# Kernel optimization log

Measured on AMD Instinct MI355X. Metric: run time of the kernel, lower is better.

The kernel has to match this reference:

```python
import jax, jax.numpy as jnp
import numpy as np

# Config (mirrors MarketBDHConfig / BDHConfig defaults used here)
B, T = 2, 512
NUM_ASSETS, IN_FEAT = 93, 4
D = 256          # n_embd
NH = 4           # n_head
MULT = 64        # mlp_internal_dim_multiplier
NL = 6           # n_layer
NI = D * MULT // NH  # per-head internal dim N = 4096
IN_DIM = NUM_ASSETS * IN_FEAT  # 372
ROPE_THETA = 2.0 ** 16
EPS = 1e-5


def _ln(x):
    # LayerNorm over last dim, elementwise_affine=False
    m = jnp.mean(x, axis=-1, keepdims=True)
    v = jnp.mean(jnp.square(x - m), axis=-1, keepdims=True)
    return (x - m) * jax.lax.rsqrt(v + EPS)


def _rope(x, cos, sin):
    # x: [B,NH,T,NI]; cos/sin: [T, NI//2] (broadcast over B,NH)
    x1, x2 = x[..., 0::2], x[..., 1::2]
    out = jnp.stack([x1 * cos - x2 * sin, x1 * sin + x2 * cos], axis=-1)
    return out.reshape(x.shape)


def setup_inputs() -> dict:
    key = jax.random.key(0)
    ks = jax.random.split(key, 9)
    s = 0.02
    return {
        "x": jax.random.normal(ks[0], (B, T, NUM_ASSETS, IN_FEAT), jnp.float32),
        "in_W": jax.random.normal(ks[1], (IN_DIM, D), jnp.float32) * s,
        "in_b": jnp.zeros((D,), jnp.float32),
        "encoder": jax.random.normal(ks[2], (NH, D, NI), jnp.float32) * s,
        "encoder_v": jax.random.normal(ks[3], (NH, D, NI), jnp.float32) * s,
        "decoder": jax.random.normal(ks[4], (NH * NI, D), jnp.float32) * s,
        "head_W": jax.random.normal(ks[5], (D, IN_DIM), jnp.float32) * s,
        "head_b": jnp.zeros((IN_DIM,), jnp.float32),
    }


def reference(x, in_W, in_b, encoder, encoder_v, decoder, head_W, head_b):
    # input projection: [B,T,N,F] -> [B,T,IN_DIM] -> [B,T,D]
    x_flat = x.reshape(B, T, IN_DIM)
    h = _ln(x_flat @ in_W + in_b)  # [B,T,D]

    # RoPE phase tables over the internal (latent) dimension
    freqs = 1.0 / (ROPE_THETA ** (jnp.arange(0, NI, 2, dtype=jnp.float32) / NI))
    phases = jnp.arange(T, dtype=jnp.float32)[:, None] * freqs[None, :]  # [T, NI/2]
    cos, sin = jnp.cos(phases), jnp.sin(phases)

    dec = decoder.reshape(NH, NI, D)  # head-major flatten matches transpose(1,2).reshape

    for _ in range(NL):
        h_res = h
        # encode + relu-sparsify: [B,NH,T,NI]
        h_sparse = jax.nn.relu(jnp.einsum('btd,hdn->bhtn', h, encoder))
        # BDH attention: linear (no softmax), K is Q, is_causal=False -> dense scores
        qr = _rope(h_sparse, cos, sin)
        scores = jnp.einsum('bhtn,bhsn->bhts', qr, qr)  # [B,NH,T,T]
        yKV = jnp.einsum('bhts,bsd->bhtd', scores, h)    # V = h broadcast over heads
        yKV = _ln(yKV)
        y_sparse = jax.nn.relu(jnp.einsum('bhtd,hdn->bhtn', yKV, encoder_v))
        xy_sparse = h_sparse * y_sparse  # multiplicative gating (dropout p=0)
        yMLP = jnp.einsum('bhtn,hnd->btd', xy_sparse, dec)
        h = _ln(h_res + _ln(yMLP))

    pred = (h @ head_W + head_b).reshape(B, T, NUM_ASSETS, IN_FEAT)
    return pred
```

## Files before the change

kernel.cpp:

```cpp
#include <hip/hip_runtime.h>
#include <math.h>

#define B_ 2
#define T_ 512
#define D_ 256
#define NH_ 4
#define NI_ 4096
#define IN_DIM_ 372
#define NL_ 6
#define EPS_ 1e-5f

typedef unsigned short u16;
typedef __attribute__((ext_vector_type(4))) float f32x4;
typedef __attribute__((ext_vector_type(8))) short bf16x8;

__device__ __forceinline__ u16 f2b(float f) {
  union { float f; unsigned u; } v; v.f = f;
  unsigned r = v.u + 0x7fffu + ((v.u >> 16) & 1u);
  return (u16)(r >> 16);
}
__device__ __forceinline__ float b2f(u16 s) {
  union { unsigned u; float f; } v; v.u = ((unsigned)s) << 16;
  return v.f;
}

__device__ __forceinline__ void gload16(const u16* g, u16* l) {
  __builtin_amdgcn_global_load_lds(
      (const __attribute__((address_space(1))) unsigned int*)g,
      (__attribute__((address_space(3))) unsigned int*)l, 16, 0, 0);
}

#define WAITV(N) asm volatile("s_waitcnt vmcnt(" #N ")" ::: "memory")

__device__ __forceinline__ float waveSum(float v) {
  #pragma unroll
  for (int o = 32; o > 0; o >>= 1) v += __shfl_xor(v, o, 64);
  return v;
}

__device__ __forceinline__ float blkSum256(float v, float* sb4) {
  #pragma unroll
  for (int o = 32; o > 0; o >>= 1) v += __shfl_down(v, o, 64);
  int w = threadIdx.x >> 6;
  __syncthreads();
  if ((threadIdx.x & 63) == 0) sb4[w] = v;
  __syncthreads();
  return sb4[0] + sb4[1] + sb4[2] + sb4[3];
}

template <int SAMEAB>
__device__ __forceinline__ void gemm128p(const u16* __restrict__ A,
                                         const u16* __restrict__ Bt,
                                         int lda, int k0, int k1,
                                         int row0, int col0,
                                         u16* smem, f32x4 acc[4][4]) {
  const int tid = threadIdx.x;
  const int lane = tid & 63;
  const int wv = tid >> 6;
  const int wr = (wv >> 1) << 6;
  const int wc = (wv & 1) << 6;
  const int frow = lane & 15;
  const int kg = lane >> 4;
  u16* Als = smem;
  u16* Bls = smem + 12288;
  #pragma unroll
  for (int m = 0; m < 4; m++)
    #pragma unroll
    for (int n = 0; n < 4; n++) {
      f32x4 z = {0.f, 0.f, 0.f, 0.f};
      acc[m][n] = z;
    }
  auto stage = [&](int k, int buf) {
    #pragma unroll
    for (int i = 0; i < 2; i++) {
      int s = tid + (i << 8);
      int r = s >> 2;
      int c = (((s & 3) ^ (r & 3)) << 3);
      gload16(A + (long)(row0 + r) * lda + k + c, Als + buf * 4096 + s * 8);
    }
    if (!SAMEAB) {
      #pragma unroll
      for (int i = 0; i < 2; i++) {
        int s = tid + (i << 8);
        int r = s >> 2;
        int c = (((s & 3) ^ (r & 3)) << 3);
        gload16(Bt + (long)(col0 + r) * lda + k + c, Bls + buf * 4096 + s * 8);
      }
    }
  };
  const int nk = (k1 - k0) >> 5;
  stage(k0, 0);
  stage(k0 + 32, 1);
  for (int i = 0; i < nk; i++) {
    if (i + 2 < nk) {
      if (SAMEAB) WAITV(2); else WAITV(4);
      __builtin_amdgcn_s_barrier();
      stage(k0 + (i + 2) * 32, (i + 2) % 3);
    } else if (i + 1 < nk) {
      if (SAMEAB) WAITV(2); else WAITV(4);
      __builtin_amdgcn_s_barrier();
    } else {
      WAITV(0);
      __builtin_amdgcn_s_barrier();
    }
    const int bi = i % 3;
    const u16* Ab = Als + bi * 4096;
    const u16* Bb = SAMEAB ? Ab : (Bls + bi * 4096);
    bf16x8 af[4], bfv[4];
    #pragma unroll
    for (int m = 0; m < 4; m++) {
      int rr = wr + m * 16 + frow;
      af[m] = *(const bf16x8*)(Ab + rr * 32 + ((kg ^ (rr & 3)) << 3));
    }
    #pragma unroll
    for (int n = 0; n < 4; n++) {
      int rr = wc + n * 16 + frow;
      bfv[n] = *(const bf16x8*)(Bb + rr * 32 + ((kg ^ (rr & 3)) << 3));
    }
    __builtin_amdgcn_s_setprio(1);
    #pragma unroll
    for (int m = 0; m < 4; m++)
      #pragma unroll
      for (int n = 0; n < 4; n++)
        acc[m][n] = __builtin_amdgcn_mfma_f32_16x16x32_bf16(af[m], bfv[n], acc[m][n], 0, 0, 0);
    __builtin_amdgcn_s_setprio(0);
  }
  __syncthreads();
}

#define EPILOG_SETUP \
  const int lane = threadIdx.x & 63; \
  const int wv = threadIdx.x >> 6; \
  const int wr = (wv >> 1) << 6, wc = (wv & 1) << 6;

#define STAGE_FULL(EXPR) \
  _Pragma("unroll") \
  for (int m = 0; m < 4; m++) \
    _Pragma("unroll") \
    for (int n = 0; n < 4; n++) \
      _Pragma("unroll") \
      for (int r = 0; r < 4; r++) { \
        int lr = wr + m * 16 + ((lane >> 4) << 2) + r; \
        int lc = wc + n * 16 + (lane & 15); \
        float _a = acc[m][n][r]; \
        smem[lr * 128 + (lc ^ (((lr >> 2) & 7) << 3))] = f2b(EXPR); \
      } \
  __syncthreads();

__device__ __forceinline__ void storeC_full(const f32x4 acc[4][4], u16* smem,
                                            u16* Cb, int ldc, int row0, int col0,
                                            int wr, int wc, int lane) {
  const int tid = threadIdx.x;
  STAGE_FULL(_a)
  #pragma unroll
  for (int i = 0; i < 8; i++) {
    int idx = i * 256 + tid;
    int lr = idx >> 4, ch = idx & 15;
    uint4 v = *(const uint4*)(smem + lr * 128 + ((ch ^ ((lr >> 2) & 7)) << 3));
    *(uint4*)(Cb + (long)(row0 + lr) * ldc + col0 + ch * 8) = v;
  }
}

#define STAGE_HALF(EXPR) \
  if (wr == h * 64) { \
    _Pragma("unroll") \
    for (int m = 0; m < 4; m++) \
      _Pragma("unroll") \
      for (int n = 0; n < 4; n++) \
        _Pragma("unroll") \
        for (int r = 0; r < 4; r++) { \
          int lr = m * 16 + ((lane >> 4) << 2) + r; \
          int lc = wc + n * 16 + (lane & 15); \
          float _a = acc[m][n][r]; \
          smem[lr * 128 + (lc ^ (((lr >> 2) & 7) << 3))] = f2b(EXPR); \
        } \
  } \
  __syncthreads();

__device__ __forceinline__ void storeC_lds(const f32x4 acc[4][4], u16* smem,
                                           u16* Cb, int ldc, int row0, int col0,
                                           int wr, int wc, int lane) {
  const int tid = threadIdx.x;
  #pragma unroll
  for (int h = 0; h < 2; h++) {
    STAGE_HALF(_a)
    #pragma unroll
    for (int i = 0; i < 4; i++) {
      int idx = i * 256 + tid;
      int lr = idx >> 4, ch = idx & 15;
      uint4 v = *(const uint4*)(smem + lr * 128 + ((ch ^ ((lr >> 2) & 7)) << 3));
      *(uint4*)(Cb + (long)(row0 + h * 64 + lr) * ldc + col0 + ch * 8) = v;
    }
    __syncthreads();
  }
}

__global__ __launch_bounds__(256)
void k_cs(unsigned* __restrict__ cs) {
  int idx = blockIdx.x * 256 + threadIdx.x;
  if (idx >= T_ * (NI_ / 2)) return;
  int t = idx >> 11;
  int k = idx & 2047;
  float freq = exp2f(-(float)k * (1.0f / 128.0f));
  float ph = (float)t * freq;
  cs[idx] = (unsigned)f2b(cosf(ph)) | ((unsigned)f2b(sinf(ph)) << 16);
}

__global__ __launch_bounds__(256)
void ktr(const float* __restrict__ src, u16* __restrict__ dst, int R, int C) {
  __shared__ float tile[64][65];
  long zoff = (long)blockIdx.z * R * C;
  int r0 = blockIdx.y * 64, c0 = blockIdx.x * 64;
  int tid = threadIdx.x;
  int tr = tid >> 4, tc4 = (tid & 15) * 4;
  #pragma unroll
  for (int i = 0; i < 4; i++) {
    int r = tr + i * 16;
    f32x4 v = *(const f32x4*)(src + zoff + (long)(r0 + r) * C + c0 + tc4);
    tile[r][tc4 + 0] = v.x; tile[r][tc4 + 1] = v.y;
    tile[r][tc4 + 2] = v.z; tile[r][tc4 + 3] = v.w;
  }
  __syncthreads();
  #pragma unroll
  for (int i = 0; i < 4; i++) {
    int c = tr + i * 16;
    ushort4 o;
    o.x = f2b(tile[tc4 + 0][c]); o.y = f2b(tile[tc4 + 1][c]);
    o.z = f2b(tile[tc4 + 2][c]); o.w = f2b(tile[tc4 + 3][c]);
    *(ushort4*)(dst + zoff + (long)(c0 + c) * R + r0 + tc4) = o;
  }
}

__global__ __launch_bounds__(256)
void ktrW(const float* __restrict__ e0, const float* __restrict__ e1,
          u16* __restrict__ d0, u16* __restrict__ d1) {
  __shared__ float tile[64][65];
  int z = blockIdx.z;
  const float* src = (z < 4) ? e0 : e1;
  u16* dst = (z < 4) ? d0 : d1;
  long zoff = (long)(z & 3) * D_ * NI_;
  int r0 = blockIdx.y * 64, c0 = blockIdx.x * 64;
  int tid = threadIdx.x;
  int tr = tid >> 4, tc4 = (tid & 15) * 4;
  #pragma unroll
  for (int i = 0; i < 4; i++) {
    int r = tr + i * 16;
    f32x4 v = *(const f32x4*)(src + zoff + (long)(r0 + r) * NI_ + c0 + tc4);
    tile[r][tc4 + 0] = v.x; tile[r][tc4 + 1] = v.y;
    tile[r][tc4 + 2] = v.z; tile[r][tc4 + 3] = v.w;
  }
  __syncthreads();
  #pragma unroll
  for (int i = 0; i < 4; i++) {
    int c = tr + i * 16;
    ushort4 o;
    o.x = f2b(tile[tc4 + 0][c]); o.y = f2b(tile[tc4 + 1][c]);
    o.z = f2b(tile[tc4 + 2][c]); o.w = f2b(tile[tc4 + 3][c]);
    *(ushort4*)(dst + zoff + (long)(c0 + c) * D_ + r0 + tc4) = o;
  }
}

__global__ __launch_bounds__(256)
void k_input(const float* __restrict__ x, const float* __restrict__ W,
             const float* __restrict__ b, float* __restrict__ hf,
             u16* __restrict__ hbf, u16* __restrict__ hT) {
  __shared__ float xr[8][IN_DIM_];
  __shared__ float sb[4];
  int bt0 = blockIdx.x * 8;
  int d = threadIdx.x;
  for (int i = d; i < 8 * IN_DIM_; i += 256)
    xr[i / IN_DIM_][i % IN_DIM_] = x[(long)bt0 * IN_DIM_ + i];
  __syncthreads();
  float acc[8];
  float bias = b[d];
  #pragma unroll
  for (int r = 0; r < 8; r++) acc[r] = bias;
  for (int k = 0; k < IN_DIM_; k++) {
    float w = W[k * D_ + d];
    #pragma unroll
    for (int r = 0; r < 8; r++) acc[r] += xr[r][k] * w;
  }
  #pragma unroll
  for (int r = 0; r < 8; r++) {
    int bt = bt0 + r;
    float mean = blkSum256(acc[r], sb) * (1.0f / D_);
    float c = acc[r] - mean;
    float var = blkSum256(c * c, sb) * (1.0f / D_);
    float out = c * rsqrtf(var + EPS_);
    hf[(long)bt * D_ + d] = out;
    hbf[(long)bt * D_ + d] = f2b(out);
    hT[((long)(bt >> 9) * D_ + d) * T_ + (bt & 511)] = f2b(out);
  }
}

__global__ __launch_bounds__(256)
void g_enc(const u16* __restrict__ hbf, const u16* __restrict__ enct,
           const unsigned* __restrict__ cs, u16* __restrict__ qr) {
  __shared__ u16 smem[24576];
  int head = blockIdx.z;
  int row0 = blockIdx.y * 128, col0 = blockIdx.x * 128;
  f32x4 acc[4][4];
  gemm128p<0>(hbf, enct + (long)head * NI_ * D_, D_, 0, D_, row0, col0, smem, acc);
  EPILOG_SETUP
  const int tid = threadIdx.x;
  STAGE_FULL(fmaxf(_a, 0.f))
  #pragma unroll
  for (int i = 0; i < 8; i++) {
    int idx = i * 256 + tid;
    int lr = idx >> 4, ch = idx & 15;
    uint4 v = *(const uint4*)(smem + lr * 128 + ((ch ^ ((lr >> 2) & 7)) << 3));
    int gr = row0 + lr;
    int b = gr >> 9, t = gr & 511;
    int gcol = col0 + ch * 8;
    uint4 csv = *(const uint4*)(cs + (long)t * (NI_ / 2) + (gcol >> 1));
    const unsigned* pv = &v.x; const unsigned* pc = &csv.x;
    unsigned o[4];
    #pragma unroll
    for (int j = 0; j < 4; j++) {
      float v0 = b2f((u16)pv[j]), v1 = b2f((u16)(pv[j] >> 16));
      float cc = b2f((u16)pc[j]), ss = b2f((u16)(pc[j] >> 16));
      o[j] = (unsigned)f2b(v0 * cc - v1 * ss) | ((unsigned)f2b(v0 * ss + v1 * cc) << 16);
    }
    long qri = (((long)(b * NH_ + head)) * T_ + t) * NI_ + gcol;
    *(uint4*)(qr + qri) = make_uint4(o[0], o[1], o[2], o[3]);
  }
}

__global__ __launch_bounds__(256)
void g_scores(const u16* __restrict__ qr, u16* __restrict__ scpb) {
  __shared__ u16 smem[24576];
  int tix = blockIdx.x;
  int by = (tix < 4) ? 0 : (tix < 7) ? 1 : (tix < 9) ? 2 : 3;
  int sub = (by == 0) ? 0 : (by == 1) ? 3 : (by == 2) ? 5 : 6;
  int bx = tix - sub;
  int z2 = blockIdx.z;
  int z = z2 >> 2, ks = z2 & 3;
  const u16* A = qr + (long)z * T_ * NI_;
  int row0 = by * 128, col0 = bx * 128;
  f32x4 acc[4][4];
  if (by == bx)
    gemm128p<1>(A, A, NI_, ks * 1024, ks * 1024 + 1024, row0, col0, smem, acc);
  else
    gemm128p<0>(A, A, NI_, ks * 1024, ks * 1024 + 1024, row0, col0, smem, acc);
  EPILOG_SETUP
  u16* Cb = scpb + (long)(ks * 8 + z) * T_ * T_;
  storeC_full(acc, smem, Cb, T_, row0, col0, wr, wc, lane);
  if (by != bx) {
    #pragma unroll
    for (int m = 0; m < 4; m++)
      #pragma unroll
      for (int n = 0; n < 4; n++) {
        int gc = col0 + wc + n * 16 + (lane & 15);
        int gr0 = row0 + wr + m * 16 + ((lane >> 4) << 2);
        uint2 o;
        o.x = (unsigned)f2b(acc[m][n][0]) | ((unsigned)f2b(acc[m][n][1]) << 16);
        o.y = (unsigned)f2b(acc[m][n][2]) | ((unsigned)f2b(acc[m][n][3]) << 16);
        *(uint2*)(Cb + (long)gc * T_ + gr0) = o;
      }
  }
}

__global__ __launch_bounds__(256)
void g_ykv(const u16* __restrict__ scpb, const u16* __restrict__ hT,
           u16* __restrict__ ykvpb) {
  __shared__ u16 smem[16384];
  u16* Als = smem;
  u16* Bls = smem + 8192;
  int z2 = blockIdx.z;
  int z = z2 >> 2, ks = z2 & 3;
  int b = z >> 2;
  int row0 = blockIdx.y * 128, col0 = blockIdx.x * 128;
  const long SL = (long)8 * T_ * T_;
  const u16* Ab = scpb + (long)z * T_ * T_;
  const u16* Bt = hT + (long)b * D_ * T_;
  const int tid = threadIdx.x;
  const int lane = tid & 63;
  const int wv = tid >> 6;
  const int wr = (wv >> 1) << 6, wc = (wv & 1) << 6;
  const int frow = lane & 15;
  const int kg = lane >> 4;
  const int sw = frow & 7;
  f32x4 acc[4][4];
  #pragma unroll
  for (int m = 0; m < 4; m++)
    #pragma unroll
    for (int n = 0; n < 4; n++) {
      f32x4 zz = {0.f, 0.f, 0.f, 0.f};
      acc[m][n] = zz;
    }
  const int ar = tid >> 1;
  const int ac0 = (tid & 1) << 2;
  for (int k = ks * 128; k < ks * 128 + 128; k += 64) {
    long gb = (long)(row0 + ar) * T_ + k;
    #pragma unroll
    for (int j = 0; j < 4; j++) {
      int jj = ac0 + j;
      long ga = gb + (jj << 3);
      uint4 p0 = *(const uint4*)(Ab + ga);
      uint4 p1 = *(const uint4*)(Ab + SL + ga);
      uint4 p2 = *(const uint4*)(Ab + 2 * SL + ga);
      uint4 p3 = *(const uint4*)(Ab + 3 * SL + ga);
      const unsigned* q0 = &p0.x; const unsigned* q1 = &p1.x;
      const unsigned* q2 = &p2.x; const unsigned* q3 = &p3.x;
      unsigned o[4];
      #pragma unroll
      for (int w = 0; w < 4; w++) {
        float lo = b2f((u16)q0[w]) + b2f((u16)q1[w]) + b2f((u16)q2[w]) + b2f((u16)q3[w]);
        float hi = b2f((u16)(q0[w] >> 16)) + b2f((u16)(q1[w] >> 16)) +
                   b2f((u16)(q2[w] >> 16)) + b2f((u16)(q3[w] >> 16));
        o[w] = (unsigned)f2b(lo) | ((unsigned)f2b(hi) << 16);
      }
      *(uint4*)(Als + ar * 64 + ((jj ^ (ar & 7)) << 3)) = make_uint4(o[0], o[1], o[2], o[3]);
    }
    #pragma unroll
    for (int i = 0; i < 4; i++) {
      int s = tid + (i << 8);
      int r = s >> 3;
      int c = (((s & 7) ^ (r & 7)) << 3);
      gload16(Bt + (long)(col0 + r) * T_ + k + c, Bls + s * 8);
    }
    __syncthreads();
    #pragma unroll
    for (int kk = 0; kk < 2; kk++) {
      const int slot = ((((kk << 2) + kg) ^ sw) << 3);
      bf16x8 af[4], bfv[4];
      #pragma unroll
      for (int m = 0; m < 4; m++)
        af[m] = *(const bf16x8*)(Als + (wr + m * 16 + frow) * 64 + slot);
      #pragma unroll
      for (int n = 0; n < 4; n++)
        bfv[n] = *(const bf16x8*)(Bls + (wc + n * 16 + frow) * 64 + slot);
      __builtin_amdgcn_s_setprio(1);
      #pragma unroll
      for (int m = 0; m < 4; m++)
        #pragma unroll
        for (int n = 0; n < 4; n++)
          acc[m][n] = __builtin_amdgcn_mfma_f32_16x16x32_bf16(af[m], bfv[n], acc[m][n], 0, 0, 0);
      __builtin_amdgcn_s_setprio(0);
    }
    __syncthreads();
  }
  storeC_lds(acc, smem, ykvpb + (long)(ks * 8 + z) * T_ * D_, D_, row0, col0, wr, wc, lane);
}

__global__ __launch_bounds__(256)
void k_lnykv(const u16* __restrict__ ykvpb, u16* __restrict__ ykvb) {
  int row = blockIdx.x * 4 + (threadIdx.x >> 6);
  int lane = threadIdx.x & 63;
  const long SL = (long)8 * T_ * D_;
  long base = (long)row * D_ + lane * 4;
  float v0 = 0.f, v1 = 0.f, v2 = 0.f, v3 = 0.f;
  #pragma unroll
  for (int p = 0; p < 4; p++) {
    uint2 w = *(const uint2*)(ykvpb + p * SL + base);
    v0 += b2f((u16)w.x); v1 += b2f((u16)(w.x >> 16));
    v2 += b2f((u16)w.y); v3 += b2f((u16)(w.y >> 16));
  }
  float mean = waveSum(v0 + v1 + v2 + v3) * (1.0f / D_);
  float c0 = v0 - mean, c1 = v1 - mean, c2 = v2 - mean, c3 = v3 - mean;
  float var = waveSum(c0 * c0 + c1 * c1 + c2 * c2 + c3 * c3) * (1.0f / D_);
  float rs = rsqrtf(var + EPS_);
  uint2 o;
  o.x = (unsigned)f2b(c0 * rs) | ((unsigned)f2b(c1 * rs) << 16);
  o.y = (unsigned)f2b(c2 * rs) | ((unsigned)f2b(c3 * rs) << 16);
  *(uint2*)(ykvb + base) = o;
}

__global__ __launch_bounds__(256)
void g_ysp(const u16* __restrict__ ykvb, const u16* __restrict__ encvt,
           const u16* __restrict__ qr, const unsigned* __restrict__ cs,
           u16* __restrict__ xy) {
  __shared__ u16 smem[24576];
  int z = blockIdx.z;
  int b = z >> 2, head = z & 3;
  int row0 = blockIdx.y * 128, col0 = blockIdx.x * 128;
  f32x4 acc[4][4];
  gemm128p<0>(ykvb + (long)z * T_ * D_, encvt + (long)head * NI_ * D_, D_,
              0, D_, row0, col0, smem, acc);
  EPILOG_SETUP
  const int tid = threadIdx.x;
  STAGE_FULL(fmaxf(_a, 0.f))
  #pragma unroll
  for (int i = 0; i < 8; i++) {
    int idx = i * 256 + tid;
    int lr = idx >> 4, ch = idx & 15;
    uint4 v = *(const uint4*)(smem + lr * 128 + ((ch ^ ((lr >> 2) & 7)) << 3));
    int t = row0 + lr;
    int gcol = col0 + ch * 8;
    uint4 qv = *(const uint4*)(qr + ((long)z * T_ + t) * NI_ + gcol);
    uint4 csv = *(const uint4*)(cs + (long)t * (NI_ / 2) + (gcol >> 1));
    const unsigned* pv = &v.x; const unsigned* pq = &qv.x; const unsigned* pc = &csv.x;
    unsigned o[4];
    #pragma unroll
    for (int j = 0; j < 4; j++) {
      float v0 = b2f((u16)pv[j]), v1 = b2f((u16)(pv[j] >> 16));
      float q0 = b2f((u16)pq[j]), q1 = b2f((u16)(pq[j] >> 16));
      float cc = b2f((u16)pc[j]), ss = b2f((u16)(pc[j] >> 16));
      float hs0 = fmaxf(cc * q0 + ss * q1, 0.f);
      float hs1 = fmaxf(cc * q1 - ss * q0, 0.f);
      o[j] = (unsigned)f2b(hs0 * v0) | ((unsigned)f2b(hs1 * v1) << 16);
    }
    long xyi = ((long)b * T_ + t) * (NH_ * NI_) + head * NI_ + gcol;
    *(uint4*)(xy + xyi) = make_uint4(o[0], o[1], o[2], o[3]);
  }
}

__global__ __launch_bounds__(256)
void g_ymlp(const u16* __restrict__ xy, const u16* __restrict__ dect,
            u16* __restrict__ ymlppb) {
  __shared__ u16 smem[24576];
  int ks = blockIdx.z;
  int row0 = blockIdx.y * 128, col0 = blockIdx.x * 128;
  f32x4 acc[4][4];
  gemm128p<0>(xy, dect, NH_ * NI_, ks * 1024, ks * 1024 + 1024, row0, col0, smem, acc);
  EPILOG_SETUP
  storeC_full(acc, smem, ymlppb + (long)ks * (B_ * T_) * D_, D_, row0, col0, wr, wc, lane);
}

__global__ __launch_bounds__(256)
void k_dln(const u16* __restrict__ ymlppb, float* __restrict__ hf,
           u16* __restrict__ hbf, u16* __restrict__ hT) {
  int bt = blockIdx.x * 4 + (threadIdx.x >> 6);
  int lane = threadIdx.x & 63;
  const long SL = (long)(B_ * T_) * D_;
  long base = (long)bt * D_ + lane * 4;
  float v0 = 0.f, v1 = 0.f, v2 = 0.f, v3 = 0.f;
  #pragma unroll
  for (int p = 0; p < 16; p++) {
    uint2 w = *(const uint2*)(ymlppb + p * SL + base);
    v0 += b2f((u16)w.x); v1 += b2f((u16)(w.x >> 16));
    v2 += b2f((u16)w.y); v3 += b2f((u16)(w.y >> 16));
  }
  float mean = waveSum(v0 + v1 + v2 + v3) * (1.0f / D_);
  float c0 = v0 - mean, c1 = v1 - mean, c2 = v2 - mean, c3 = v3 - mean;
  float var = waveSum(c0 * c0 + c1 * c1 + c2 * c2 + c3 * c3) * (1.0f / D_);
  float rs = rsqrtf(var + EPS_);
  f32x4 hv = *(const f32x4*)(hf + base);
  float w0 = hv.x + c0 * rs, w1 = hv.y + c1 * rs;
  float w2 = hv.z + c2 * rs, w3 = hv.w + c3 * rs;
  float m2 = waveSum(w0 + w1 + w2 + w3) * (1.0f / D_);
  float e0 = w0 - m2, e1 = w1 - m2, e2 = w2 - m2, e3 = w3 - m2;
  float va2 = waveSum(e0 * e0 + e1 * e1 + e2 * e2 + e3 * e3) * (1.0f / D_);
  float rs2 = rsqrtf(va2 + EPS_);
  float o0 = e0 * rs2, o1 = e1 * rs2, o2 = e2 * rs2, o3 = e3 * rs2;
  f32x4 of = {o0, o1, o2, o3};
  *(f32x4*)(hf + base) = of;
  uint2 ob;
  ob.x = (unsigned)f2b(o0) | ((unsigned)f2b(o1) << 16);
  ob.y = (unsigned)f2b(o2) | ((unsigned)f2b(o3) << 16);
  *(uint2*)(hbf + base) = ob;
  int b = bt >> 9, t = bt & 511;
  int d0 = lane * 4;
  hT[((long)b * D_ + d0 + 0) * T_ + t] = f2b(o0);
  hT[((long)b * D_ + d0 + 1) * T_ + t] = f2b(o1);
  hT[((long)b * D_ + d0 + 2) * T_ + t] = f2b(o2);
  hT[((long)b * D_ + d0 + 3) * T_ + t] = f2b(o3);
}

__global__ __launch_bounds__(384)
void k_head(const float* __restrict__ h, const float* __restrict__ W,
            const float* __restrict__ bb, float* __restrict__ out) {
  __shared__ float hr[8][D_];
  int bt0 = blockIdx.x * 8;
  int j = threadIdx.x;
  for (int i = j; i < 8 * D_; i += 384)
    hr[i >> 8][i & 255] = h[(long)bt0 * D_ + i];
  __syncthreads();
  if (j < IN_DIM_) {
    float acc[8];
    float bias = bb[j];
    #pragma unroll
    for (int r = 0; r < 8; r++) acc[r] = bias;
    for (int d2 = 0; d2 < D_; d2++) {
      float w = W[(long)d2 * IN_DIM_ + j];
      #pragma unroll
      for (int r = 0; r < 8; r++) acc[r] += hr[r][d2] * w;
    }
    #pragma unroll
    for (int r = 0; r < 8; r++)
      out[(long)(bt0 + r) * IN_DIM_ + j] = acc[r];
  }
}

extern "C" void kernel_launch(void* const* d_in, const int* in_sizes, int n_in,
                              void* d_out, int out_size, void* d_ws, size_t ws_size,
                              hipStream_t stream) {
  const float* x    = (const float*)d_in[0];
  const float* in_W = (const float*)d_in[1];
  const float* in_b = (const float*)d_in[2];
  const float* enc  = (const float*)d_in[3];
  const float* encv = (const float*)d_in[4];
  const float* dec  = (const float*)d_in[5];
  const float* hW   = (const float*)d_in[6];
  const float* hb   = (const float*)d_in[7];
  float* out = (float*)d_out;

  char* p = (char*)d_ws;
  auto alloc = [&](size_t bytes) { char* r = p; p += (bytes + 255) & ~(size_t)255; return r; };
  unsigned* cs   = (unsigned*)alloc((size_t)T_ * (NI_ / 2) * 4);
  float* hf      = (float*)alloc((size_t)B_ * T_ * D_ * 4);
  u16*   hbf     = (u16*)  alloc((size_t)B_ * T_ * D_ * 2);
  u16*   hT      = (u16*)  alloc((size_t)B_ * D_ * T_ * 2);
  u16*   enct    = (u16*)  alloc((size_t)NH_ * D_ * NI_ * 2);
  u16*   encvt   = (u16*)  alloc((size_t)NH_ * D_ * NI_ * 2);
  u16*   dect    = (u16*)  alloc((size_t)NH_ * NI_ * D_ * 2);
  u16*   qr      = (u16*)  alloc((size_t)B_ * NH_ * T_ * NI_ * 2);
  u16*   xy      = (u16*)  alloc((size_t)B_ * T_ * NH_ * NI_ * 2);
  u16*   scpb    = (u16*)  alloc((size_t)4 * 8 * T_ * T_ * 2);
  u16*   ykvpb   = (u16*)  alloc((size_t)4 * 8 * T_ * D_ * 2);
  u16*   ykvb    = (u16*)  alloc((size_t)8 * T_ * D_ * 2);
  u16*   ymlppb  = (u16*)  alloc((size_t)16 * B_ * T_ * D_ * 2);

  k_cs<<<dim3(4096), dim3(256), 0, stream>>>(cs);
  ktrW<<<dim3(NI_ / 64, D_ / 64, 8), dim3(256), 0, stream>>>(enc, encv, enct, encvt);
  ktr<<<dim3(D_ / 64, (NH_ * NI_) / 64, 1), dim3(256), 0, stream>>>(dec, dect, NH_ * NI_, D_);
  k_input<<<dim3(B_ * T_ / 8), dim3(256), 0, stream>>>(x, in_W, in_b, hf, hbf, hT);

  for (int l = 0; l < NL_; l++) {
    g_enc<<<dim3(32, 8, 4), dim3(256), 0, stream>>>(hbf, enct, cs, qr);
    g_scores<<<dim3(10, 1, 32), dim3(256), 0, stream>>>(qr, scpb);
    g_ykv<<<dim3(2, 4, 32), dim3(256), 0, stream>>>(scpb, hT, ykvpb);
    k_lnykv<<<dim3(1024), dim3(256), 0, stream>>>(ykvpb, ykvb);
    g_ysp<<<dim3(32, 4, 8), dim3(256), 0, stream>>>(ykvb, encvt, qr, cs, xy);
    g_ymlp<<<dim3(2, 8, 16), dim3(256), 0, stream>>>(xy, dect, ymlppb);
    k_dln<<<dim3(256), dim3(256), 0, stream>>>(ymlppb, hf, hbf, hT);
  }

  k_head<<<dim3(B_ * T_ / 8), dim3(384), 0, stream>>>(hf, hW, hb, out);
}
```

Before: 754.8 us.

## Double split-K for scores and MLP GEMMs, merge prep kernels, split-K input/head

```diff
diff --git a/kernel.cpp b/kernel.cpp
--- a/kernel.cpp
+++ b/kernel.cpp
@@ -196,27 +196,41 @@
 }
 
 __global__ __launch_bounds__(256)
-void k_cs(unsigned* __restrict__ cs) {
-  int idx = blockIdx.x * 256 + threadIdx.x;
-  if (idx >= T_ * (NI_ / 2)) return;
-  int t = idx >> 11;
-  int k = idx & 2047;
-  float freq = exp2f(-(float)k * (1.0f / 128.0f));
-  float ph = (float)t * freq;
-  cs[idx] = (unsigned)f2b(cosf(ph)) | ((unsigned)f2b(sinf(ph)) << 16);
-}
-
-__global__ __launch_bounds__(256)
-void ktr(const float* __restrict__ src, u16* __restrict__ dst, int R, int C) {
+void k_pre(const float* __restrict__ enc, const float* __restrict__ encv,
+           const float* __restrict__ dec, u16* __restrict__ enct,
+           u16* __restrict__ encvt, u16* __restrict__ dect,
+           unsigned* __restrict__ cs) {
   __shared__ float tile[64][65];
-  long zoff = (long)blockIdx.z * R * C;
-  int r0 = blockIdx.y * 64, c0 = blockIdx.x * 64;
+  int id = blockIdx.x;
   int tid = threadIdx.x;
+  if (id < 4096) {
+    int idx = id * 256 + tid;
+    int t = idx >> 11;
+    int k = idx & 2047;
+    float freq = exp2f(-(float)k * (1.0f / 128.0f));
+    float ph = (float)t * freq;
+    cs[idx] = (unsigned)f2b(cosf(ph)) | ((unsigned)f2b(sinf(ph)) << 16);
+    return;
+  }
+  const float* src; u16* dst; long zoff; int r0, c0, Rd, Cd;
+  if (id < 6144) {
+    int q = id - 4096;
+    int x = q & 63, y = (q >> 6) & 3, z = q >> 8;
+    src = (z < 4) ? enc : encv;
+    dst = (z < 4) ? enct : encvt;
+    zoff = (long)(z & 3) * D_ * NI_;
+    r0 = y * 64; c0 = x * 64; Rd = D_; Cd = NI_;
+  } else {
+    int q = id - 6144;
+    int x = q & 3, y = q >> 2;
+    src = dec; dst = dect; zoff = 0;
+    r0 = y * 64; c0 = x * 64; Rd = NH_ * NI_; Cd = D_;
+  }
   int tr = tid >> 4, tc4 = (tid & 15) * 4;
   #pragma unroll
   for (int i = 0; i < 4; i++) {
     int r = tr + i * 16;
-    f32x4 v = *(const f32x4*)(src + zoff + (long)(r0 + r) * C + c0 + tc4);
+    f32x4 v = *(const f32x4*)(src + zoff + (long)(r0 + r) * Cd + c0 + tc4);
     tile[r][tc4 + 0] = v.x; tile[r][tc4 + 1] = v.y;
     tile[r][tc4 + 2] = v.z; tile[r][tc4 + 3] = v.w;
   }
@@ -227,36 +241,7 @@
     ushort4 o;
     o.x = f2b(tile[tc4 + 0][c]); o.y = f2b(tile[tc4 + 1][c]);
     o.z = f2b(tile[tc4 + 2][c]); o.w = f2b(tile[tc4 + 3][c]);
-    *(ushort4*)(dst + zoff + (long)(c0 + c) * R + r0 + tc4) = o;
-  }
-}
-
-__global__ __launch_bounds__(256)
-void ktrW(const float* __restrict__ e0, const float* __restrict__ e1,
-          u16* __restrict__ d0, u16* __restrict__ d1) {
-  __shared__ float tile[64][65];
-  int z = blockIdx.z;
-  const float* src = (z < 4) ? e0 : e1;
-  u16* dst = (z < 4) ? d0 : d1;
-  long zoff = (long)(z & 3) * D_ * NI_;
-  int r0 = blockIdx.y * 64, c0 = blockIdx.x * 64;
-  int tid = threadIdx.x;
-  int tr = tid >> 4, tc4 = (tid & 15) * 4;
-  #pragma unroll
-  for (int i = 0; i < 4; i++) {
-    int r = tr + i * 16;
-    f32x4 v = *(const f32x4*)(src + zoff + (long)(r0 + r) * NI_ + c0 + tc4);
-    tile[r][tc4 + 0] = v.x; tile[r][tc4 + 1] = v.y;
-    tile[r][tc4 + 2] = v.z; tile[r][tc4 + 3] = v.w;
-  }
-  __syncthreads();
-  #pragma unroll
-  for (int i = 0; i < 4; i++) {
-    int c = tr + i * 16;
-    ushort4 o;
-    o.x = f2b(tile[tc4 + 0][c]); o.y = f2b(tile[tc4 + 1][c]);
-    o.z = f2b(tile[tc4 + 2][c]); o.w = f2b(tile[tc4 + 3][c]);
-    *(ushort4*)(dst + zoff + (long)(c0 + c) * D_ + r0 + tc4) = o;
+    *(ushort4*)(dst + zoff + (long)(c0 + c) * Rd + r0 + tc4) = o;
   }
 }
 
@@ -264,29 +249,39 @@
 void k_input(const float* __restrict__ x, const float* __restrict__ W,
              const float* __restrict__ b, float* __restrict__ hf,
              u16* __restrict__ hbf, u16* __restrict__ hT) {
-  __shared__ float xr[8][IN_DIM_];
+  __shared__ float xr[2][IN_DIM_];
+  __shared__ float part[4][2][D_];
   __shared__ float sb[4];
-  int bt0 = blockIdx.x * 8;
-  int d = threadIdx.x;
-  for (int i = d; i < 8 * IN_DIM_; i += 256)
+  int bt0 = blockIdx.x * 2;
+  int tid = threadIdx.x;
+  int wv = tid >> 6, l = tid & 63;
+  for (int i = tid; i < 2 * IN_DIM_; i += 256)
     xr[i / IN_DIM_][i % IN_DIM_] = x[(long)bt0 * IN_DIM_ + i];
   __syncthreads();
-  float acc[8];
-  float bias = b[d];
-  #pragma unroll
-  for (int r = 0; r < 8; r++) acc[r] = bias;
-  for (int k = 0; k < IN_DIM_; k++) {
-    float w = W[k * D_ + d];
-    #pragma unroll
-    for (int r = 0; r < 8; r++) acc[r] += xr[r][k] * w;
-  }
-  #pragma unroll
-  for (int r = 0; r < 8; r++) {
-    int bt = bt0 + r;
-    float mean = blkSum256(acc[r], sb) * (1.0f / D_);
-    float c = acc[r] - mean;
+  float a00 = 0, a01 = 0, a02 = 0, a03 = 0;
+  float a10 = 0, a11 = 0, a12 = 0, a13 = 0;
+  int kbeg = wv * 93, kend = kbeg + 93;
+  for (int k = kbeg; k < kend; k++) {
+    const float* Wr = W + (long)k * D_ + l;
+    float w0 = Wr[0], w1 = Wr[64], w2 = Wr[128], w3 = Wr[192];
+    float x0 = xr[0][k], x1 = xr[1][k];
+    a00 += x0 * w0; a01 += x0 * w1; a02 += x0 * w2; a03 += x0 * w3;
+    a10 += x1 * w0; a11 += x1 * w1; a12 += x1 * w2; a13 += x1 * w3;
+  }
+  part[wv][0][l] = a00; part[wv][0][l + 64] = a01;
+  part[wv][0][l + 128] = a02; part[wv][0][l + 192] = a03;
+  part[wv][1][l] = a10; part[wv][1][l + 64] = a11;
+  part[wv][1][l + 128] = a12; part[wv][1][l + 192] = a13;
+  __syncthreads();
+  int d = tid;
+  #pragma unroll
+  for (int r = 0; r < 2; r++) {
+    float s = part[0][r][d] + part[1][r][d] + part[2][r][d] + part[3][r][d] + b[d];
+    float mean = blkSum256(s, sb) * (1.0f / D_);
+    float c = s - mean;
     float var = blkSum256(c * c, sb) * (1.0f / D_);
     float out = c * rsqrtf(var + EPS_);
+    int bt = bt0 + r;
     hf[(long)bt * D_ + d] = out;
     hbf[(long)bt * D_ + d] = f2b(out);
     hT[((long)(bt >> 9) * D_ + d) * T_ + (bt & 511)] = f2b(out);
@@ -334,14 +329,14 @@
   int sub = (by == 0) ? 0 : (by == 1) ? 3 : (by == 2) ? 5 : 6;
   int bx = tix - sub;
   int z2 = blockIdx.z;
-  int z = z2 >> 2, ks = z2 & 3;
+  int z = z2 >> 3, ks = z2 & 7;
   const u16* A = qr + (long)z * T_ * NI_;
   int row0 = by * 128, col0 = bx * 128;
   f32x4 acc[4][4];
   if (by == bx)
-    gemm128p<1>(A, A, NI_, ks * 1024, ks * 1024 + 1024, row0, col0, smem, acc);
+    gemm128p<1>(A, A, NI_, ks * 512, ks * 512 + 512, row0, col0, smem, acc);
   else
-    gemm128p<0>(A, A, NI_, ks * 1024, ks * 1024 + 1024, row0, col0, smem, acc);
+    gemm128p<0>(A, A, NI_, ks * 512, ks * 512 + 512, row0, col0, smem, acc);
   EPILOG_SETUP
   u16* Cb = scpb + (long)(ks * 8 + z) * T_ * T_;
   storeC_full(acc, smem, Cb, T_, row0, col0, wr, wc, lane);
@@ -396,20 +391,22 @@
     for (int j = 0; j < 4; j++) {
       int jj = ac0 + j;
       long ga = gb + (jj << 3);
-      uint4 p0 = *(const uint4*)(Ab + ga);
-      uint4 p1 = *(const uint4*)(Ab + SL + ga);
-      uint4 p2 = *(const uint4*)(Ab + 2 * SL + ga);
-      uint4 p3 = *(const uint4*)(Ab + 3 * SL + ga);
-      const unsigned* q0 = &p0.x; const unsigned* q1 = &p1.x;
-      const unsigned* q2 = &p2.x; const unsigned* q3 = &p3.x;
+      float lo[4] = {0.f, 0.f, 0.f, 0.f};
+      float hi[4] = {0.f, 0.f, 0.f, 0.f};
+      #pragma unroll
+      for (int pp = 0; pp < 8; pp++) {
+        uint4 pv = *(const uint4*)(Ab + pp * SL + ga);
+        const unsigned* q = &pv.x;
+        #pragma unroll
+        for (int w = 0; w < 4; w++) {
+          lo[w] += b2f((u16)q[w]);
+          hi[w] += b2f((u16)(q[w] >> 16));
+        }
+      }
       unsigned o[4];
       #pragma unroll
-      for (int w = 0; w < 4; w++) {
-        float lo = b2f((u16)q0[w]) + b2f((u16)q1[w]) + b2f((u16)q2[w]) + b2f((u16)q3[w]);
-        float hi = b2f((u16)(q0[w] >> 16)) + b2f((u16)(q1[w] >> 16)) +
-                   b2f((u16)(q2[w] >> 16)) + b2f((u16)(q3[w] >> 16));
-        o[w] = (unsigned)f2b(lo) | ((unsigned)f2b(hi) << 16);
-      }
+      for (int w = 0; w < 4; w++)
+        o[w] = (unsigned)f2b(lo[w]) | ((unsigned)f2b(hi[w]) << 16);
       *(uint4*)(Als + ar * 64 + ((jj ^ (ar & 7)) << 3)) = make_uint4(o[0], o[1], o[2], o[3]);
     }
     #pragma unroll
@@ -512,7 +509,7 @@
   int ks = blockIdx.z;
   int row0 = blockIdx.y * 128, col0 = blockIdx.x * 128;
   f32x4 acc[4][4];
-  gemm128p<0>(xy, dect, NH_ * NI_, ks * 1024, ks * 1024 + 1024, row0, col0, smem, acc);
+  gemm128p<0>(xy, dect, NH_ * NI_, ks * 512, ks * 512 + 512, row0, col0, smem, acc);
   EPILOG_SETUP
   storeC_full(acc, smem, ymlppb + (long)ks * (B_ * T_) * D_, D_, row0, col0, wr, wc, lane);
 }
@@ -526,7 +523,7 @@
   long base = (long)bt * D_ + lane * 4;
   float v0 = 0.f, v1 = 0.f, v2 = 0.f, v3 = 0.f;
   #pragma unroll
-  for (int p = 0; p < 16; p++) {
+  for (int p = 0; p < 32; p++) {
     uint2 w = *(const uint2*)(ymlppb + p * SL + base);
     v0 += b2f((u16)w.x); v1 += b2f((u16)(w.x >> 16));
     v2 += b2f((u16)w.y); v3 += b2f((u16)(w.y >> 16));
@@ -557,28 +554,47 @@
   hT[((long)b * D_ + d0 + 3) * T_ + t] = f2b(o3);
 }
 
-__global__ __launch_bounds__(384)
+__global__ __launch_bounds__(256)
 void k_head(const float* __restrict__ h, const float* __restrict__ W,
             const float* __restrict__ bb, float* __restrict__ out) {
-  __shared__ float hr[8][D_];
-  int bt0 = blockIdx.x * 8;
-  int j = threadIdx.x;
-  for (int i = j; i < 8 * D_; i += 384)
+  __shared__ float hr[2][D_];
+  __shared__ float part[4][2][384];
+  int bt0 = blockIdx.x * 2;
+  int tid = threadIdx.x;
+  int wv = tid >> 6, l = tid & 63;
+  for (int i = tid; i < 2 * D_; i += 256)
     hr[i >> 8][i & 255] = h[(long)bt0 * D_ + i];
   __syncthreads();
-  if (j < IN_DIM_) {
-    float acc[8];
-    float bias = bb[j];
-    #pragma unroll
-    for (int r = 0; r < 8; r++) acc[r] = bias;
-    for (int d2 = 0; d2 < D_; d2++) {
-      float w = W[(long)d2 * IN_DIM_ + j];
-      #pragma unroll
-      for (int r = 0; r < 8; r++) acc[r] += hr[r][d2] * w;
-    }
-    #pragma unroll
-    for (int r = 0; r < 8; r++)
-      out[(long)(bt0 + r) * IN_DIM_ + j] = acc[r];
+  float a0[6] = {0.f, 0.f, 0.f, 0.f, 0.f, 0.f};
+  float a1[6] = {0.f, 0.f, 0.f, 0.f, 0.f, 0.f};
+  int kbeg = wv * 64, kend = kbeg + 64;
+  for (int k = kbeg; k < kend; k++) {
+    float x0 = hr[0][k], x1 = hr[1][k];
+    const float* Wr = W + (long)k * IN_DIM_;
+    #pragma unroll
+    for (int jj = 0; jj < 6; jj++) {
+      int j = l + jj * 64;
+      float w = (j < IN_DIM_) ? Wr[j] : 0.f;
+      a0[jj] += x0 * w;
+      a1[jj] += x1 * w;
+    }
+  }
+  #pragma unroll
+  for (int jj = 0; jj < 6; jj++) {
+    int j = l + jj * 64;
+    part[wv][0][j] = a0[jj];
+    part[wv][1][j] = a1[jj];
+  }
+  __syncthreads();
+  #pragma unroll
+  for (int pass = 0; pass < 2; pass++) {
+    int j = tid + pass * 256;
+    if (j < IN_DIM_) {
+      float s0 = part[0][0][j] + part[1][0][j] + part[2][0][j] + part[3][0][j] + bb[j];
+      float s1 = part[0][1][j] + part[1][1][j] + part[2][1][j] + part[3][1][j] + bb[j];
+      out[(long)bt0 * IN_DIM_ + j] = s0;
+      out[(long)(bt0 + 1) * IN_DIM_ + j] = s1;
+    }
   }
 }
 
@@ -606,25 +622,23 @@
   u16*   dect    = (u16*)  alloc((size_t)NH_ * NI_ * D_ * 2);
   u16*   qr      = (u16*)  alloc((size_t)B_ * NH_ * T_ * NI_ * 2);
   u16*   xy      = (u16*)  alloc((size_t)B_ * T_ * NH_ * NI_ * 2);
-  u16*   scpb    = (u16*)  alloc((size_t)4 * 8 * T_ * T_ * 2);
+  u16*   scpb    = (u16*)  alloc((size_t)8 * 8 * T_ * T_ * 2);
   u16*   ykvpb   = (u16*)  alloc((size_t)4 * 8 * T_ * D_ * 2);
   u16*   ykvb    = (u16*)  alloc((size_t)8 * T_ * D_ * 2);
-  u16*   ymlppb  = (u16*)  alloc((size_t)16 * B_ * T_ * D_ * 2);
-
-  k_cs<<<dim3(4096), dim3(256), 0, stream>>>(cs);
-  ktrW<<<dim3(NI_ / 64, D_ / 64, 8), dim3(256), 0, stream>>>(enc, encv, enct, encvt);
-  ktr<<<dim3(D_ / 64, (NH_ * NI_) / 64, 1), dim3(256), 0, stream>>>(dec, dect, NH_ * NI_, D_);
-  k_input<<<dim3(B_ * T_ / 8), dim3(256), 0, stream>>>(x, in_W, in_b, hf, hbf, hT);
+  u16*   ymlppb  = (u16*)  alloc((size_t)32 * B_ * T_ * D_ * 2);
+
+  k_pre<<<dim3(7168), dim3(256), 0, stream>>>(enc, encv, dec, enct, encvt, dect, cs);
+  k_input<<<dim3(B_ * T_ / 2), dim3(256), 0, stream>>>(x, in_W, in_b, hf, hbf, hT);
 
   for (int l = 0; l < NL_; l++) {
     g_enc<<<dim3(32, 8, 4), dim3(256), 0, stream>>>(hbf, enct, cs, qr);
-    g_scores<<<dim3(10, 1, 32), dim3(256), 0, stream>>>(qr, scpb);
+    g_scores<<<dim3(10, 1, 64), dim3(256), 0, stream>>>(qr, scpb);
     g_ykv<<<dim3(2, 4, 32), dim3(256), 0, stream>>>(scpb, hT, ykvpb);
     k_lnykv<<<dim3(1024), dim3(256), 0, stream>>>(ykvpb, ykvb);
     g_ysp<<<dim3(32, 4, 8), dim3(256), 0, stream>>>(ykvb, encvt, qr, cs, xy);
-    g_ymlp<<<dim3(2, 8, 16), dim3(256), 0, stream>>>(xy, dect, ymlppb);
+    g_ymlp<<<dim3(2, 8, 32), dim3(256), 0, stream>>>(xy, dect, ymlppb);
     k_dln<<<dim3(256), dim3(256), 0, stream>>>(ymlppb, hf, hbf, hT);
   }
 
-  k_head<<<dim3(B_ * T_ / 8), dim3(384), 0, stream>>>(hf, hW, hb, out);
-}
+  k_head<<<dim3(B_ * T_ / 2), dim3(256), 0, stream>>>(hf, hW, hb, out);
+}
```

Result: slower. 818.0 us (+8.4%).
